# Kernel optimization log

Hardware: AMD Instinct MI355X
Metric: run time of the kernel (lower is better)

Reference implementation:

```python
import jax, jax.numpy as jnp
import numpy as np

# Static config (matches init_kwargs)
B, H, W, C = 8, 80, 60, 512
WS, SHIFT = 10, 5
NH = 16
HD = C // NH  # 32
L = WS * WS  # 100 tokens per window
NW = (H // WS) * (W // WS)  # 48 windows per image
EPS = 1e-5


def _relative_position_index():
    coords = np.stack(np.meshgrid(np.arange(WS), np.arange(WS), indexing='ij'))  # (2,WS,WS)
    flat = coords.reshape(2, -1)  # (2, L)
    rel = flat[:, :, None] - flat[:, None, :]  # (2, L, L)
    rel = rel.transpose(1, 2, 0)  # (L, L, 2)
    rel[:, :, 0] += WS - 1
    rel[:, :, 1] += WS - 1
    rel[:, :, 0] *= 2 * WS - 1
    return rel.sum(-1)  # (L, L) indices into (2*WS-1)^2 table


def _attn_mask():
    # Swin shift mask: label 3x3 regions, tokens in different regions cannot attend.
    img = np.zeros((H, W), dtype=np.float32)
    slices = (slice(0, -WS), slice(-WS, -SHIFT), slice(-SHIFT, None))
    cnt = 0
    for hs in slices:
        for ws_ in slices:
            img[hs, ws_] = cnt
            cnt += 1
    mw = img.reshape(H // WS, WS, W // WS, WS).transpose(0, 2, 1, 3).reshape(NW, L)
    diff = mw[:, None, :] - mw[:, :, None]  # (NW, L, L)
    return np.where(diff != 0, -100.0, 0.0).astype(np.float32)


REL_IDX = jnp.asarray(_relative_position_index())
ATTN_MASK = jnp.asarray(_attn_mask())


def layernorm(x, g, b):
    mu = jnp.mean(x, axis=-1, keepdims=True)
    var = jnp.mean(jnp.square(x - mu), axis=-1, keepdims=True)
    return (x - mu) * jax.lax.rsqrt(var + EPS) * g + b


def setup_inputs() -> dict:
    key = jax.random.key(0)
    ks = jax.random.split(key, 8)
    s = 0.02
    return {
        'hidden_states': jax.random.normal(ks[0], (B, H * W, C), jnp.float32),
        'ln1_g': jnp.ones((C,), jnp.float32),
        'ln1_b': jnp.zeros((C,), jnp.float32),
        'wq': jax.random.normal(ks[1], (C, C), jnp.float32) * s,
        'bq': jnp.zeros((C,), jnp.float32),
        'wk': jax.random.normal(ks[2], (C, C), jnp.float32) * s,
        'bk': jnp.zeros((C,), jnp.float32),
        'wv': jax.random.normal(ks[3], (C, C), jnp.float32) * s,
        'bv': jnp.zeros((C,), jnp.float32),
        'wo': jax.random.normal(ks[4], (C, C), jnp.float32) * s,
        'bo': jnp.zeros((C,), jnp.float32),
        'rel_bias_table': jax.random.normal(ks[5], ((2 * WS - 1) ** 2, NH), jnp.float32) * s,
        'ln2_g': jnp.ones((C,), jnp.float32),
        'ln2_b': jnp.zeros((C,), jnp.float32),
        'w1': jax.random.normal(ks[6], (C, 4 * C), jnp.float32) * s,
        'b1': jnp.zeros((4 * C,), jnp.float32),
        'w2': jax.random.normal(ks[7], (4 * C, C), jnp.float32) * s,
        'b2': jnp.zeros((C,), jnp.float32),
    }


def reference(hidden_states, ln1_g, ln1_b, wq, bq, wk, bk, wv, bv, wo, bo,
              rel_bias_table, ln2_g, ln2_b, w1, b1, w2, b2):
    shortcut = hidden_states  # (B, H*W, C)
    x = layernorm(hidden_states, ln1_g, ln1_b).reshape(B, H, W, C)
    # cyclic shift (H, W divisible by WS -> no padding needed)
    x = jnp.roll(x, (-SHIFT, -SHIFT), axis=(1, 2))
    # window partition -> (B*NW, L, C)
    win = x.reshape(B, H // WS, WS, W // WS, WS, C).transpose(0, 1, 3, 2, 4, 5)
    win = win.reshape(B * NW, L, C)
    # multi-head attention within windows
    q = (win @ wq + bq).reshape(-1, L, NH, HD).transpose(0, 2, 1, 3)
    k = (win @ wk + bk).reshape(-1, L, NH, HD).transpose(0, 2, 1, 3)
    v = (win @ wv + bv).reshape(-1, L, NH, HD).transpose(0, 2, 1, 3)
    scores = jnp.einsum('bhqd,bhkd->bhqk', q, k) / np.sqrt(HD).astype(np.float32)
    bias = rel_bias_table[REL_IDX.reshape(-1)].reshape(L, L, NH).transpose(2, 0, 1)
    scores = scores + bias[None]  # (B*NW, NH, L, L)
    scores = scores.reshape(B, NW, NH, L, L) + ATTN_MASK[None, :, None]
    attn = jax.nn.softmax(scores.reshape(B * NW, NH, L, L), axis=-1)
    ctx = jnp.einsum('bhqk,bhkd->bhqd', attn, v).transpose(0, 2, 1, 3).reshape(B * NW, L, C)
    out = ctx @ wo + bo
    # window reverse + un-shift
    out = out.reshape(B, H // WS, W // WS, WS, WS, C).transpose(0, 1, 3, 2, 4, 5)
    out = out.reshape(B, H, W, C)
    out = jnp.roll(out, (SHIFT, SHIFT), axis=(1, 2)).reshape(B, H * W, C)
    hs = shortcut + out
    # FFN with post-residual layernorm input
    y = layernorm(hs, ln2_g, ln2_b)
    y = jax.nn.gelu(y @ w1 + b1, approximate=False) @ w2 + b2
    return hs + y
```

## Files before the change

### kernel.cpp

```cpp
#include <hip/hip_runtime.h>
#include <math.h>

typedef unsigned short u16;
typedef unsigned int u32;
typedef __bf16 bf16x8 __attribute__((ext_vector_type(8)));
typedef float f32x4 __attribute__((ext_vector_type(4)));

__device__ __forceinline__ float b2f(u16 u) { return __uint_as_float(((u32)u) << 16); }
__device__ __forceinline__ u16 f2b(float f) {
    u32 x = __float_as_uint(f);
    return (u16)((x + 0x7FFFu + ((x >> 16) & 1u)) >> 16);
}
__device__ __forceinline__ void load8f(const float* p, size_t idx, float* o) {
    const float4* q = (const float4*)(p + idx);
    float4 a = q[0], b = q[1];
    o[0]=a.x; o[1]=a.y; o[2]=a.z; o[3]=a.w; o[4]=b.x; o[5]=b.y; o[6]=b.z; o[7]=b.w;
}
__device__ __forceinline__ void gld16(const void* g, void* l) {
    __builtin_amdgcn_global_load_lds(
        (const __attribute__((address_space(1))) u32*)g,
        (__attribute__((address_space(3))) u32*)l, 16, 0, 0);
}

__global__ __launch_bounds__(256) void transpose_k(const float* __restrict__ Win, u16* __restrict__ Wt,
                                                   int Kd, int Nd, float scale) {
    __shared__ u16 tile[32][33];
    int tx = threadIdx.x & 31, ty = threadIdx.x >> 5;
    int k0 = blockIdx.x << 5, n0 = blockIdx.y << 5;
#pragma unroll
    for (int r = 0; r < 4; r++)
        tile[ty + 8 * r][tx] = f2b(Win[(size_t)(k0 + ty + 8 * r) * Nd + (n0 + tx)] * scale);
    __syncthreads();
#pragma unroll
    for (int r = 0; r < 4; r++)
        Wt[(size_t)(n0 + ty + 8 * r) * Kd + (k0 + tx)] = tile[tx][ty + 8 * r];
}

__global__ __launch_bounds__(256) void biascat_k(const float* __restrict__ bq, const float* __restrict__ bk,
                                                 const float* __restrict__ bv, float* __restrict__ o) {
    int i = blockIdx.x * 256 + threadIdx.x;
    float v = (i < 512) ? bq[i] * 0.17677669529663689f : (i < 1024 ? bk[i - 512] : bv[i - 1024]);
    o[i] = v;
}

__global__ __launch_bounds__(256) void ln1win_k(const float* __restrict__ x, const float* __restrict__ g,
                                                const float* __restrict__ bta, u16* __restrict__ win) {
    int wave = threadIdx.x >> 6, lane = threadIdx.x & 63;
    int token = blockIdx.x * 4 + wave;
    int b = token / 4800, rem = token - b * 4800;
    int h = rem / 60, w = rem - h * 60;
    int hr = h + 75; if (hr >= 80) hr -= 80;
    int wr = w + 55; if (wr >= 60) wr -= 60;
    int widx = (hr / 10) * 6 + (wr / 10);
    int l = (hr - (hr / 10) * 10) * 10 + (wr - (wr / 10) * 10);
    size_t dstrow = ((size_t)b * 48 + widx) * 100 + l;
    int c0 = lane * 8;
    float v[8]; load8f(x, (size_t)token * 512 + c0, v);
    float s = 0.f, s2 = 0.f;
#pragma unroll
    for (int e = 0; e < 8; e++) { s += v[e]; s2 += v[e] * v[e]; }
#pragma unroll
    for (int o = 32; o > 0; o >>= 1) { s += __shfl_xor(s, o); s2 += __shfl_xor(s2, o); }
    float mean = s * (1.0f / 512.0f);
    float var = fmaxf(s2 * (1.0f / 512.0f) - mean * mean, 0.0f);
    float rstd = rsqrtf(var + 1e-5f);
    uint4 o4; u16* ou = (u16*)&o4;
#pragma unroll
    for (int e = 0; e < 8; e++)
        ou[e] = f2b((v[e] - mean) * rstd * g[c0 + e] + bta[c0 + e]);
    *(uint4*)(win + dstrow * 512 + c0) = o4;
}

__global__ __launch_bounds__(256) void resid2_k(const float* __restrict__ shortcut, const u16* __restrict__ attn_out,
                                                const float* __restrict__ g, const float* __restrict__ bta,
                                                u16* __restrict__ hs, u16* __restrict__ ln2y) {
    int wave = threadIdx.x >> 6, lane = threadIdx.x & 63;
    int token = blockIdx.x * 4 + wave;
    int b = token / 4800, rem = token - b * 4800;
    int h = rem / 60, w = rem - h * 60;
    int hr = h + 75; if (hr >= 80) hr -= 80;
    int wr = w + 55; if (wr >= 60) wr -= 60;
    int widx = (hr / 10) * 6 + (wr / 10);
    int l = (hr - (hr / 10) * 10) * 10 + (wr - (wr / 10) * 10);
    size_t arow = ((size_t)b * 48 + widx) * 100 + l;
    int c0 = lane * 8;
    float sv[8]; load8f(shortcut, (size_t)token * 512 + c0, sv);
    uint4 da = *(const uint4*)(attn_out + arow * 512 + c0);
    const u16* au = (const u16*)&da;
    float hv[8]; float s = 0.f, s2 = 0.f;
    uint4 oh; u16* ohu = (u16*)&oh;
#pragma unroll
    for (int e = 0; e < 8; e++) {
        hv[e] = sv[e] + b2f(au[e]);
        s += hv[e]; s2 += hv[e] * hv[e];
        ohu[e] = f2b(hv[e]);
    }
    *(uint4*)(hs + (size_t)token * 512 + c0) = oh;
#pragma unroll
    for (int off = 32; off > 0; off >>= 1) { s += __shfl_xor(s, off); s2 += __shfl_xor(s2, off); }
    float mean = s * (1.0f / 512.0f);
    float var = fmaxf(s2 * (1.0f / 512.0f) - mean * mean, 0.0f);
    float rstd = rsqrtf(var + 1e-5f);
    uint4 oy; u16* oyu = (u16*)&oy;
#pragma unroll
    for (int e = 0; e < 8; e++)
        oyu[e] = f2b((hv[e] - mean) * rstd * g[c0 + e] + bta[c0 + e]);
    *(uint4*)(ln2y + (size_t)token * 512 + c0) = oy;
}

template <int EPI, int OF32, int QKV>
__global__ __launch_bounds__(512, 2) void gemm_k(const u16* __restrict__ A, const u16* __restrict__ Bt,
                                                 const float* __restrict__ bias, const u16* __restrict__ res,
                                                 void* __restrict__ C0, void* __restrict__ C1, void* __restrict__ C2,
                                                 int M, int N, int K) {
    __shared__ __align__(16) u16 As[2][256 * 64];
    __shared__ __align__(16) u16 Bs[2][256 * 64];
    int tid = threadIdx.x;
    int wave = tid >> 6, lane = tid & 63;
    int l15 = lane & 15, quad = lane >> 4;
    int wr = wave >> 2, wc = wave & 3;

    int gy = gridDim.y;
    int nwg = gridDim.x * gy;
    int lid = blockIdx.x + blockIdx.y * gridDim.x;
    int xcd = lid & 7, loc = lid >> 3;
    int q8 = nwg >> 3, r8 = nwg & 7;
    int wg = (xcd < r8 ? xcd * (q8 + 1) : r8 * (q8 + 1) + (xcd - r8) * q8) + loc;
    int bn = wg % gy, bm = wg / gy;

    f32x4 acc[8][4];
#pragma unroll
    for (int i = 0; i < 8; i++)
#pragma unroll
        for (int j = 0; j < 4; j++) acc[i][j] = (f32x4){0.f, 0.f, 0.f, 0.f};

    const u16* Ab = A + (size_t)(bm * 256) * K;
    const u16* Bb = Bt + (size_t)(bn * 256) * K;

    int lrow = lane >> 3;
    int cg = (lane & 7) ^ lrow;
    size_t gOff = (size_t)(wave * 8 + lrow) * K + cg * 8;
    int e = l15 & 7;
    int xk0 = (quad ^ e) * 8;
    int xk1 = xk0 ^ 32;
    int aRow = (wr * 128 + l15) * 64;
    int bRow = (wc * 64 + l15) * 64;

    auto STAGE_A = [&](int b, int kt, int i) {
        gld16(Ab + (size_t)(i * 64) * K + kt + gOff, &As[b][(i * 64 + wave * 8) * 64]);
    };
    auto STAGE_B = [&](int b, int kt, int j) {
        gld16(Bb + (size_t)(j * 64) * K + kt + gOff, &Bs[b][(j * 64 + wave * 8) * 64]);
    };

#define MM16(MH)                                                                     \
    do {                                                                             \
        __builtin_amdgcn_s_setprio(1);                                               \
        _Pragma("unroll") for (int i_ = 0; i_ < 4; i_++)                             \
            _Pragma("unroll") for (int n_ = 0; n_ < 4; n_++)                         \
                acc[(MH) * 4 + i_][n_] = __builtin_amdgcn_mfma_f32_16x16x32_bf16(    \
                    a_[i_], b_[n_], acc[(MH) * 4 + i_][n_], 0, 0, 0);                \
        __builtin_amdgcn_s_setprio(0);                                               \
    } while (0)

    int T = K >> 6;
    STAGE_B(0, 0, 0); STAGE_B(0, 0, 1);
    STAGE_B(0, 0, 2); STAGE_B(0, 0, 3);
    STAGE_A(0, 0, 0); STAGE_A(0, 0, 2);
    STAGE_A(0, 0, 1); STAGE_A(0, 0, 3);

#pragma unroll 1
    for (int t = 0; t < T; t++) {
        int cur = t & 1, nxt = cur ^ 1;
        int ktn = (t + 1) << 6;
        bool pf = (t + 1 < T);
        bf16x8 a_[4], b_[4];
        if (pf) {
            STAGE_B(nxt, ktn, 0); STAGE_B(nxt, ktn, 1);
            asm volatile("s_waitcnt vmcnt(4)" ::: "memory");
        } else {
            asm volatile("s_waitcnt vmcnt(2)" ::: "memory");
        }
        __builtin_amdgcn_s_barrier();
        asm volatile("" ::: "memory");
#pragma unroll
        for (int n = 0; n < 4; n++) b_[n] = *(const bf16x8*)(&Bs[cur][bRow + n * 1024 + xk0]);
#pragma unroll
        for (int i = 0; i < 4; i++) a_[i] = *(const bf16x8*)(&As[cur][aRow + i * 1024 + xk0]);
        MM16(0);
        if (pf) {
            STAGE_B(nxt, ktn, 2); STAGE_B(nxt, ktn, 3);
            asm volatile("s_waitcnt vmcnt(4)" ::: "memory");
        } else {
            asm volatile("s_waitcnt vmcnt(0)" ::: "memory");
        }
        __builtin_amdgcn_s_barrier();
        asm volatile("" ::: "memory");
#pragma unroll
        for (int i = 0; i < 4; i++) a_[i] = *(const bf16x8*)(&As[cur][aRow + (4 + i) * 1024 + xk0]);
        MM16(1);
        if (pf) { STAGE_A(nxt, ktn, 0); STAGE_A(nxt, ktn, 2); }
#pragma unroll
        for (int n = 0; n < 4; n++) b_[n] = *(const bf16x8*)(&Bs[cur][bRow + n * 1024 + xk1]);
#pragma unroll
        for (int i = 0; i < 4; i++) a_[i] = *(const bf16x8*)(&As[cur][aRow + i * 1024 + xk1]);
        MM16(0);
        if (pf) { STAGE_A(nxt, ktn, 1); STAGE_A(nxt, ktn, 3); }
#pragma unroll
        for (int i = 0; i < 4; i++) a_[i] = *(const bf16x8*)(&As[cur][aRow + (4 + i) * 1024 + xk1]);
        asm volatile("s_waitcnt lgkmcnt(0)" ::: "memory");
        __builtin_amdgcn_sched_barrier(0);
        __builtin_amdgcn_s_barrier();
        asm volatile("" ::: "memory");
        MM16(1);
    }
#undef MM16

    u16* Cd = (u16*)C0;
    if (QKV) {
        int sel = bn >> 1;
        Cd = (sel == 0) ? (u16*)C0 : (sel == 1) ? (u16*)C1 : (u16*)C2;
    }
#pragma unroll
    for (int m = 0; m < 8; m++) {
        int row0 = bm * 256 + wr * 128 + m * 16 + quad * 4;
#pragma unroll
        for (int n = 0; n < 4; n++) {
            int colg = bn * 256 + wc * 64 + n * 16 + l15;
            int col = QKV ? (colg & 511) : colg;
            float bv = bias[colg];
#pragma unroll
            for (int rr = 0; rr < 4; rr++) {
                int row = row0 + rr;
                float v = acc[m][n][rr] + bv;
                if (EPI == 1) {
                    float zz = 1.5957691216f * (v + 0.044715f * v * v * v);
                    float tt = 1.0f - 2.0f / (__expf(zz) + 1.0f);
                    v = 0.5f * v * (1.0f + tt);
                }
                if (EPI == 2) v += b2f(res[(size_t)row * 512 + col]);
                if (OF32) ((float*)Cd)[(size_t)row * N + col] = v;
                else      ((u16*)Cd)[(size_t)row * N + col] = f2b(v);
            }
        }
    }
}

__global__ __launch_bounds__(256) void biasprep_k(const float* __restrict__ table, u16* __restrict__ biasM) {
    int idx = blockIdx.x * 256 + threadIdx.x;
    int k = idx % 112;
    int t = idx / 112;
    int q = t % 100; t /= 100;
    int head = t & 15, wt = t >> 4;
    float v;
    if (k >= 100) {
        v = -1e30f;
    } else {
        int qi = q / 10, qj = q - qi * 10;
        int ki = k / 10, kj = k - ki * 10;
        int rel = (qi - ki) * 19 + (qj - kj) + 180;
        v = table[rel * 16 + head];
        int rq = ((wt & 2) ? (qi < 5 ? 4 : 8) : 0) + ((wt & 1) ? (qj < 5 ? 1 : 2) : 0);
        int rk = ((wt & 2) ? (ki < 5 ? 4 : 8) : 0) + ((wt & 1) ? (kj < 5 ? 1 : 2) : 0);
        if (rq != rk) v -= 100.0f;
    }
    biasM[idx] = f2b(v);
}

__global__ __launch_bounds__(256, 3) void attn_mfma_k(const u16* __restrict__ Q, const u16* __restrict__ Km,
                                                      const u16* __restrict__ V, const u16* __restrict__ biasM,
                                                      u16* __restrict__ ctx) {
    __shared__ __align__(16) u16 lds[4 * 6144];
    int tid = threadIdx.x;
    int wave = tid >> 6, lane = tid & 63;
    int l15 = lane & 15, quad = lane >> 4;
    int bid = blockIdx.x;
    int win = bid >> 2;
    int head = ((bid & 3) << 2) + wave;
    int w48 = win % 48;
    int wh = w48 / 6, ww = w48 - wh * 6;
    int wtype = ((wh == 7) ? 2 : 0) + ((ww == 5) ? 1 : 0);
    size_t base = (size_t)win * 51200 + head * 32;
    u16* Vt = lds + wave * 6144;
    u16* Pl = Vt + 4096;
    const u16* bptr = biasM + (size_t)(wtype * 16 + head) * 11200;

    {
        uint4 z = {0u, 0u, 0u, 0u};
#pragma unroll
        for (int r = 0; r < 2; r++) {
            int c = r * 64 + lane;
            int d = c >> 2, seg = c & 3;
            int k0 = 96 + seg * 8;
            *(uint4*)(Vt + d * 128 + (k0 ^ ((d & 7) << 3))) = z;
        }
        uint2 z2 = {0u, 0u};
        *(uint2*)(Pl + l15 * 128 + ((112 + quad * 4) ^ ((l15 & 7) << 3))) = z2;
    }
#pragma unroll
    for (int r = 0; r < 2; r++) {
        int k = r * 64 + lane;
        if (k < 100) {
            const uint4* vp = (const uint4*)(V + base + (size_t)k * 512);
#pragma unroll
            for (int c = 0; c < 4; c++) {
                uint4 dv = vp[c];
                const u16* e = (const u16*)&dv;
#pragma unroll
                for (int t = 0; t < 8; t++) {
                    int d = c * 8 + t;
                    Vt[d * 128 + (k ^ ((d & 7) << 3))] = e[t];
                }
            }
        }
    }
    bf16x8 kf[7];
#pragma unroll
    for (int i = 0; i < 7; i++) {
        int kr = i * 16 + l15; if (kr > 99) kr = 99;
        kf[i] = *(const bf16x8*)(Km + base + (size_t)kr * 512 + quad * 8);
    }
    bf16x8 vf[2][4];
#pragma unroll
    for (int it = 0; it < 2; it++)
#pragma unroll
        for (int ks = 0; ks < 4; ks++) {
            int D = it * 16 + l15;
            vf[it][ks] = *(const bf16x8*)(Vt + D * 128 + ((ks * 32 + quad * 8) ^ ((D & 7) << 3)));
        }

#pragma unroll 1
    for (int j = 0; j < 7; j++) {
        int q = j * 16 + l15;
        int qc = q > 99 ? 99 : q;
        bf16x8 qf = *(const bf16x8*)(Q + base + (size_t)qc * 512 + quad * 8);
        f32x4 s[7];
#pragma unroll
        for (int i = 0; i < 7; i++) {
            uint2 bb = *(const uint2*)(bptr + (size_t)qc * 112 + i * 16 + quad * 4);
            const u16* be = (const u16*)&bb;
            s[i][0] = b2f(be[0]); s[i][1] = b2f(be[1]);
            s[i][2] = b2f(be[2]); s[i][3] = b2f(be[3]);
        }
#pragma unroll
        for (int i = 0; i < 7; i++)
            s[i] = __builtin_amdgcn_mfma_f32_16x16x32_bf16(kf[i], qf, s[i], 0, 0, 0);
        float m = -1e30f;
#pragma unroll
        for (int i = 0; i < 7; i++)
#pragma unroll
            for (int rr = 0; rr < 4; rr++) m = fmaxf(m, s[i][rr]);
        m = fmaxf(m, __shfl_xor(m, 16));
        m = fmaxf(m, __shfl_xor(m, 32));
        float l = 0.f;
#pragma unroll
        for (int i = 0; i < 7; i++)
#pragma unroll
            for (int rr = 0; rr < 4; rr++) { s[i][rr] = __expf(s[i][rr] - m); l += s[i][rr]; }
        l += __shfl_xor(l, 16);
        l += __shfl_xor(l, 32);
#pragma unroll
        for (int i = 0; i < 7; i++) {
            u32 lo, hi;
            asm("v_cvt_pk_bf16_f32 %0, %1, %2" : "=v"(lo) : "v"(s[i][0]), "v"(s[i][1]));
            asm("v_cvt_pk_bf16_f32 %0, %1, %2" : "=v"(hi) : "v"(s[i][2]), "v"(s[i][3]));
            uint2 w; w.x = lo; w.y = hi;
            *(uint2*)(Pl + l15 * 128 + ((i * 16 + quad * 4) ^ ((l15 & 7) << 3))) = w;
        }
        f32x4 o0 = (f32x4){0.f, 0.f, 0.f, 0.f};
        f32x4 o1 = (f32x4){0.f, 0.f, 0.f, 0.f};
#pragma unroll
        for (int ks = 0; ks < 4; ks++) {
            bf16x8 pf = *(const bf16x8*)(Pl + l15 * 128 + ((ks * 32 + quad * 8) ^ ((l15 & 7) << 3)));
            o0 = __builtin_amdgcn_mfma_f32_16x16x32_bf16(vf[0][ks], pf, o0, 0, 0, 0);
            o1 = __builtin_amdgcn_mfma_f32_16x16x32_bf16(vf[1][ks], pf, o1, 0, 0, 0);
        }
        float inv = 1.0f / l;
        if (q < 100) {
            u16* cp = ctx + base + (size_t)q * 512;
            {
                float a0 = o0[0]*inv, a1 = o0[1]*inv, a2 = o0[2]*inv, a3 = o0[3]*inv;
                u32 lo, hi;
                asm("v_cvt_pk_bf16_f32 %0, %1, %2" : "=v"(lo) : "v"(a0), "v"(a1));
                asm("v_cvt_pk_bf16_f32 %0, %1, %2" : "=v"(hi) : "v"(a2), "v"(a3));
                uint2 w; w.x = lo; w.y = hi;
                *(uint2*)(cp + quad * 4) = w;
            }
            {
                float a0 = o1[0]*inv, a1 = o1[1]*inv, a2 = o1[2]*inv, a3 = o1[3]*inv;
                u32 lo, hi;
                asm("v_cvt_pk_bf16_f32 %0, %1, %2" : "=v"(lo) : "v"(a0), "v"(a1));
                asm("v_cvt_pk_bf16_f32 %0, %1, %2" : "=v"(hi) : "v"(a2), "v"(a3));
                uint2 w; w.x = lo; w.y = hi;
                *(uint2*)(cp + 16 + quad * 4) = w;
            }
        }
    }
}

extern "C" void kernel_launch(void* const* d_in, const int* in_sizes, int n_in,
                              void* d_out, int out_size, void* d_ws, size_t ws_size,
                              hipStream_t stream) {
    const float* hidden = (const float*)d_in[0];
    const float* ln1_g  = (const float*)d_in[1];
    const float* ln1_b  = (const float*)d_in[2];
    const float* wq = (const float*)d_in[3];  const float* bq = (const float*)d_in[4];
    const float* wk = (const float*)d_in[5];  const float* bk = (const float*)d_in[6];
    const float* wv = (const float*)d_in[7];  const float* bv = (const float*)d_in[8];
    const float* wo = (const float*)d_in[9];  const float* bo = (const float*)d_in[10];
    const float* rel = (const float*)d_in[11];
    const float* ln2_g = (const float*)d_in[12];
    const float* ln2_b = (const float*)d_in[13];
    const float* w1 = (const float*)d_in[14]; const float* b1 = (const float*)d_in[15];
    const float* w2 = (const float*)d_in[16]; const float* b2 = (const float*)d_in[17];

    const size_t NTC = 38400ull * 512;
    u16* ws = (u16*)d_ws;
    u16* R0 = ws;
    u16* R1 = ws + NTC;
    u16* Rh = ws + 2 * NTC;
    u16* wqt = ws + 3 * NTC;
    u16* wkt = wqt + 512 * 512;
    u16* wvt = wkt + 512 * 512;
    u16* wot = wvt + 512 * 512;
    u16* w1t = wot + 512 * 512;
    u16* w2t = w1t + 1048576;
    float* qkvb = (float*)(w2t + 1048576);
    u16* dlo = (u16*)d_out;
    u16* biasM = dlo + NTC;
    float* outp = (float*)d_out;

    const float SC = 0.17677669529663689f;

    transpose_k<<<dim3(16, 16), 256, 0, stream>>>(wq, wqt, 512, 512, SC);
    transpose_k<<<dim3(16, 16), 256, 0, stream>>>(wk, wkt, 512, 512, 1.0f);
    transpose_k<<<dim3(16, 16), 256, 0, stream>>>(wv, wvt, 512, 512, 1.0f);
    transpose_k<<<dim3(16, 16), 256, 0, stream>>>(wo, wot, 512, 512, 1.0f);
    transpose_k<<<dim3(16, 64), 256, 0, stream>>>(w1, w1t, 512, 2048, 1.0f);
    transpose_k<<<dim3(64, 16), 256, 0, stream>>>(w2, w2t, 2048, 512, 1.0f);
    biascat_k<<<6, 256, 0, stream>>>(bq, bk, bv, qkvb);
    biasprep_k<<<2800, 256, 0, stream>>>(rel, biasM);

    ln1win_k<<<9600, 256, 0, stream>>>(hidden, ln1_g, ln1_b, R0 );

    gemm_k<0, 0, 1><<<dim3(150, 6), 512, 0, stream>>>(R0, wqt, qkvb, nullptr,
                                                      R1 , Rh , dlo , 38400, 512, 512);

    attn_mfma_k<<<1536, 256, 0, stream>>>(R1, Rh, dlo, biasM, R0 );

    gemm_k<0, 0, 0><<<dim3(150, 2), 512, 0, stream>>>(R0, wot, bo, nullptr,
                                                      R1 , nullptr, nullptr, 38400, 512, 512);

    resid2_k<<<9600, 256, 0, stream>>>(hidden, R1, ln2_g, ln2_b, Rh , dlo );

    for (int mc = 1; mc >= 0; mc--) {
        size_t roff = (size_t)mc * 19200 * 512;
        gemm_k<1, 0, 0><<<dim3(75, 8), 512, 0, stream>>>(dlo + roff, w1t, b1, nullptr,
                                                         R0 , nullptr, nullptr, 19200, 2048, 512);
        gemm_k<2, 1, 0><<<dim3(75, 2), 512, 0, stream>>>(R0, w2t, b2, Rh + roff,
                                                         outp + roff, nullptr, nullptr, 19200, 512, 2048);
    }
}
```

Before: 752.3 us.

## Add 128x128 triple-buffered GEMM for N=512 outputs and simplify 256 GEMM prefetch

```diff
diff --git a/kernel.cpp b/kernel.cpp
--- a/kernel.cpp
+++ b/kernel.cpp
@@ -109,10 +109,10 @@
 }
 
 template <int EPI, int OF32, int QKV>
-__global__ __launch_bounds__(512, 2) void gemm_k(const u16* __restrict__ A, const u16* __restrict__ Bt,
-                                                 const float* __restrict__ bias, const u16* __restrict__ res,
-                                                 void* __restrict__ C0, void* __restrict__ C1, void* __restrict__ C2,
-                                                 int M, int N, int K) {
+__global__ __launch_bounds__(512, 2) void gemm256_k(const u16* __restrict__ A, const u16* __restrict__ Bt,
+                                                    const float* __restrict__ bias, const u16* __restrict__ res,
+                                                    void* __restrict__ C0, void* __restrict__ C1, void* __restrict__ C2,
+                                                    int M, int N, int K) {
     __shared__ __align__(16) u16 As[2][256 * 64];
     __shared__ __align__(16) u16 Bs[2][256 * 64];
     int tid = threadIdx.x;
@@ -151,6 +151,10 @@
     };
     auto STAGE_B = [&](int b, int kt, int j) {
         gld16(Bb + (size_t)(j * 64) * K + kt + gOff, &Bs[b][(j * 64 + wave * 8) * 64]);
+    };
+    auto STAGE8 = [&](int b, int kt) {
+        STAGE_B(b, kt, 0); STAGE_B(b, kt, 1); STAGE_B(b, kt, 2); STAGE_B(b, kt, 3);
+        STAGE_A(b, kt, 0); STAGE_A(b, kt, 1); STAGE_A(b, kt, 2); STAGE_A(b, kt, 3);
     };
 
 #define MM16(MH)                                                                     \
@@ -164,48 +168,32 @@
     } while (0)
 
     int T = K >> 6;
-    STAGE_B(0, 0, 0); STAGE_B(0, 0, 1);
-    STAGE_B(0, 0, 2); STAGE_B(0, 0, 3);
-    STAGE_A(0, 0, 0); STAGE_A(0, 0, 2);
-    STAGE_A(0, 0, 1); STAGE_A(0, 0, 3);
-
+    STAGE8(0, 0);
 #pragma unroll 1
     for (int t = 0; t < T; t++) {
         int cur = t & 1, nxt = cur ^ 1;
-        int ktn = (t + 1) << 6;
-        bool pf = (t + 1 < T);
-        bf16x8 a_[4], b_[4];
-        if (pf) {
-            STAGE_B(nxt, ktn, 0); STAGE_B(nxt, ktn, 1);
-            asm volatile("s_waitcnt vmcnt(4)" ::: "memory");
+        if (t + 1 < T) {
+            STAGE8(nxt, (t + 1) << 6);
+            asm volatile("s_waitcnt vmcnt(8)" ::: "memory");
         } else {
-            asm volatile("s_waitcnt vmcnt(2)" ::: "memory");
+            asm volatile("s_waitcnt vmcnt(0)" ::: "memory");
         }
         __builtin_amdgcn_s_barrier();
         asm volatile("" ::: "memory");
+        bf16x8 a_[4], b_[4];
 #pragma unroll
         for (int n = 0; n < 4; n++) b_[n] = *(const bf16x8*)(&Bs[cur][bRow + n * 1024 + xk0]);
 #pragma unroll
         for (int i = 0; i < 4; i++) a_[i] = *(const bf16x8*)(&As[cur][aRow + i * 1024 + xk0]);
         MM16(0);
-        if (pf) {
-            STAGE_B(nxt, ktn, 2); STAGE_B(nxt, ktn, 3);
-            asm volatile("s_waitcnt vmcnt(4)" ::: "memory");
-        } else {
-            asm volatile("s_waitcnt vmcnt(0)" ::: "memory");
-        }
-        __builtin_amdgcn_s_barrier();
-        asm volatile("" ::: "memory");
 #pragma unroll
         for (int i = 0; i < 4; i++) a_[i] = *(const bf16x8*)(&As[cur][aRow + (4 + i) * 1024 + xk0]);
         MM16(1);
-        if (pf) { STAGE_A(nxt, ktn, 0); STAGE_A(nxt, ktn, 2); }
 #pragma unroll
         for (int n = 0; n < 4; n++) b_[n] = *(const bf16x8*)(&Bs[cur][bRow + n * 1024 + xk1]);
 #pragma unroll
         for (int i = 0; i < 4; i++) a_[i] = *(const bf16x8*)(&As[cur][aRow + i * 1024 + xk1]);
         MM16(0);
-        if (pf) { STAGE_A(nxt, ktn, 1); STAGE_A(nxt, ktn, 3); }
 #pragma unroll
         for (int i = 0; i < 4; i++) a_[i] = *(const bf16x8*)(&As[cur][aRow + (4 + i) * 1024 + xk1]);
         asm volatile("s_waitcnt lgkmcnt(0)" ::: "memory");
@@ -233,6 +221,101 @@
             for (int rr = 0; rr < 4; rr++) {
                 int row = row0 + rr;
                 float v = acc[m][n][rr] + bv;
+                if (EPI == 1) {
+                    float zz = 1.5957691216f * (v + 0.044715f * v * v * v);
+                    float tt = 1.0f - 2.0f / (__expf(zz) + 1.0f);
+                    v = 0.5f * v * (1.0f + tt);
+                }
+                if (EPI == 2) v += b2f(res[(size_t)row * 512 + col]);
+                if (OF32) ((float*)Cd)[(size_t)row * N + col] = v;
+                else      ((u16*)Cd)[(size_t)row * N + col] = f2b(v);
+            }
+        }
+    }
+}
+
+template <int EPI, int OF32>
+__global__ __launch_bounds__(256) void gemm128_k(const u16* __restrict__ A, const u16* __restrict__ Bt,
+                                                 const float* __restrict__ bias, const u16* __restrict__ res,
+                                                 void* __restrict__ C, int M, int N, int K) {
+    __shared__ __align__(16) u16 As[3][128 * 32];
+    __shared__ __align__(16) u16 Bs[3][128 * 32];
+    int tid = threadIdx.x;
+    int wave = tid >> 6, lane = tid & 63;
+    int l15 = lane & 15, quad = lane >> 4;
+    int lq = lane >> 2, lr = lane & 3;
+    int wm = (wave >> 1) * 64, wn = (wave & 1) * 64;
+
+    int gy = gridDim.y;
+    int nwg = gridDim.x * gy;
+    int lid = blockIdx.x + blockIdx.y * gridDim.x;
+    int xcd = lid & 7, loc = lid >> 3;
+    int q8 = nwg >> 3, r8 = nwg & 7;
+    int wg = (xcd < r8 ? xcd * (q8 + 1) : r8 * (q8 + 1) + (xcd - r8) * q8) + loc;
+    int bn = wg % gy, bm = wg / gy;
+
+    f32x4 acc[4][4];
+#pragma unroll
+    for (int i = 0; i < 4; i++)
+#pragma unroll
+        for (int j = 0; j < 4; j++) acc[i][j] = (f32x4){0.f, 0.f, 0.f, 0.f};
+
+    const u16* Ab = A + (size_t)(bm * 128) * K;
+    const u16* Bb = Bt + (size_t)(bn * 128) * K;
+
+    int cgs = (lr ^ (lq & 3)) * 8;
+    int xrd = (quad ^ (l15 & 3)) * 8;
+
+    int T = K >> 5;
+    auto STAGE = [&](int b, int t) {
+        int kt = t << 5;
+#pragma unroll
+        for (int h = 0; h < 2; h++) {
+            int r = h * 64 + wave * 16 + lq;
+            gld16(Ab + (size_t)r * K + kt + cgs, &As[b][(h * 64 + wave * 16) * 32]);
+            gld16(Bb + (size_t)r * K + kt + cgs, &Bs[b][(h * 64 + wave * 16) * 32]);
+        }
+    };
+
+    STAGE(0, 0);
+    STAGE(1, 1);
+    for (int t = 0; t < T; t++) {
+        int cb = t % 3;
+        if (t + 2 < T) STAGE((t + 2) % 3, t + 2);
+        if (t + 2 < T)      asm volatile("s_waitcnt vmcnt(8)" ::: "memory");
+        else if (t + 1 < T) asm volatile("s_waitcnt vmcnt(4)" ::: "memory");
+        else                asm volatile("s_waitcnt vmcnt(0)" ::: "memory");
+        __builtin_amdgcn_s_barrier();
+        asm volatile("" ::: "memory");
+        bf16x8 af[4], bfr[4];
+#pragma unroll
+        for (int x = 0; x < 4; x++) {
+            af[x]  = *(const bf16x8*)(&As[cb][(wm + x * 16 + l15) * 32 + xrd]);
+            bfr[x] = *(const bf16x8*)(&Bs[cb][(wn + x * 16 + l15) * 32 + xrd]);
+        }
+        asm volatile("s_waitcnt lgkmcnt(0)" ::: "memory");
+        __builtin_amdgcn_sched_barrier(0);
+        __builtin_amdgcn_s_barrier();
+        asm volatile("" ::: "memory");
+#pragma unroll
+        for (int i = 0; i < 4; i++)
+#pragma unroll
+            for (int j = 0; j < 4; j++)
+                acc[i][j] = __builtin_amdgcn_mfma_f32_16x16x32_bf16(af[i], bfr[j], acc[i][j], 0, 0, 0);
+    }
+
+    u16* Cd = (u16*)C;
+#pragma unroll
+    for (int i = 0; i < 4; i++) {
+        int row0 = bm * 128 + wm + i * 16 + quad * 4;
+#pragma unroll
+        for (int j = 0; j < 4; j++) {
+            int col = bn * 128 + wn + j * 16 + l15;
+            float bv = bias[col];
+#pragma unroll
+            for (int rr = 0; rr < 4; rr++) {
+                int row = row0 + rr;
+                float v = acc[i][j][rr] + bv;
                 if (EPI == 1) {
                     float zz = 1.5957691216f * (v + 0.044715f * v * v * v);
                     float tt = 1.0f - 2.0f / (__expf(zz) + 1.0f);
@@ -443,21 +526,21 @@
 
     ln1win_k<<<9600, 256, 0, stream>>>(hidden, ln1_g, ln1_b, R0 );
 
-    gemm_k<0, 0, 1><<<dim3(150, 6), 512, 0, stream>>>(R0, wqt, qkvb, nullptr,
-                                                      R1 , Rh , dlo , 38400, 512, 512);
+    gemm256_k<0, 0, 1><<<dim3(150, 6), 512, 0, stream>>>(R0, wqt, qkvb, nullptr,
+                                                         R1 , Rh , dlo , 38400, 512, 512);
 
     attn_mfma_k<<<1536, 256, 0, stream>>>(R1, Rh, dlo, biasM, R0 );
 
-    gemm_k<0, 0, 0><<<dim3(150, 2), 512, 0, stream>>>(R0, wot, bo, nullptr,
-                                                      R1 , nullptr, nullptr, 38400, 512, 512);
+    gemm128_k<0, 0><<<dim3(300, 4), 256, 0, stream>>>(R0, wot, bo, nullptr,
+                                                      R1 , 38400, 512, 512);
 
     resid2_k<<<9600, 256, 0, stream>>>(hidden, R1, ln2_g, ln2_b, Rh , dlo );
 
     for (int mc = 1; mc >= 0; mc--) {
         size_t roff = (size_t)mc * 19200 * 512;
-        gemm_k<1, 0, 0><<<dim3(75, 8), 512, 0, stream>>>(dlo + roff, w1t, b1, nullptr,
-                                                         R0 , nullptr, nullptr, 19200, 2048, 512);
-        gemm_k<2, 1, 0><<<dim3(75, 2), 512, 0, stream>>>(R0, w2t, b2, Rh + roff,
-                                                         outp + roff, nullptr, nullptr, 19200, 512, 2048);
-    }
-}
+        gemm256_k<1, 0, 0><<<dim3(75, 8), 512, 0, stream>>>(dlo + roff, w1t, b1, nullptr,
+                                                            R0 , nullptr, nullptr, 19200, 2048, 512);
+        gemm128_k<2, 1><<<dim3(150, 4), 256, 0, stream>>>(R0, w2t, b2, Rh + roff,
+                                                          outp + roff, 19200, 512, 2048);
+    }
+}
```

After: 729.5 us. 3.0% less time.
